# Performance work log

Hardware: AMD Instinct MI355X
Metric: run time of the kernel (lower is better)

The kernel has to match this reference:

```python
import jax, jax.numpy as jnp
import numpy as np

FPFM = 256.0
B = 2097152
C = 32


def _integerize(v, scale):
    # Mirrors ArmInt.set_param_from_float: round-half-away-from-zero to int,
    # stored back as float (pure_int=False path).
    fv = v * scale
    fv = fv + jnp.sign(fv) * 0.5
    return jnp.trunc(fv)  # trunc toward zero == torch .to(int32)


def setup_inputs() -> dict:
    key = jax.random.key(0)
    ks = jax.random.split(key, 8)
    x = jax.random.normal(ks[0], (B, C), dtype=jnp.float32)
    # float-domain params (small, residual-friendly), then integerized
    w0 = _integerize(jax.random.normal(ks[1], (C, C), jnp.float32) * 0.05, FPFM)
    b0 = _integerize(jax.random.normal(ks[2], (C,), jnp.float32) * 0.05, FPFM * FPFM)
    w1 = _integerize(jax.random.normal(ks[3], (C, C), jnp.float32) * 0.05, FPFM)
    b1 = _integerize(jax.random.normal(ks[4], (C,), jnp.float32) * 0.05, FPFM * FPFM)
    w_out = _integerize(jax.random.normal(ks[5], (2, C), jnp.float32) * 0.05, FPFM)
    b_out = _integerize(jax.random.normal(ks[6], (2,), jnp.float32) * 0.05, FPFM * FPFM)
    return {"x": x, "w0": w0, "b0": b0, "w1": w1, "b1": b1,
            "w_out": w_out, "b_out": b_out}


def _arm_layer(h, W, b, residual):
    # F.linear + optional residual scaled by FPFM
    xx = h @ W.T + b
    if residual:
        xx = xx + h * FPFM
    # emulated integer rounding: add sign*FPFM/2, divide, trunc toward zero
    xx = xx + jnp.sign(xx) * (FPFM / 2.0)
    # where(xx<0, -(-xx/f), xx/f) is identity in float; trunc matches .to(int32)
    return jnp.trunc(xx / FPFM)


def reference(x, w0, b0, w1, b1, w_out, b_out):
    h = x * FPFM  # fixed-point lift (pure_int=False: stays float)
    h = jax.nn.relu(_arm_layer(h, w0, b0, True))
    h = jax.nn.relu(_arm_layer(h, w1, b1, True))
    h = _arm_layer(h, w_out, b_out, False)
    raw = h / FPFM  # [B, 2]
    mu = raw[:, 0]
    log_scale = raw[:, 1]
    scale = jnp.exp(jnp.clip(log_scale - 4.0, -4.6, 5.0))
    return mu, scale, log_scale
```

## Files before the change

### kernel.cpp

```cpp
#include <hip/hip_runtime.h>
#include <math.h>


typedef __attribute__((ext_vector_type(8))) short bf16x8;
typedef __attribute__((ext_vector_type(4))) float f32x4;

#define MFMA16(A, B, C) __builtin_amdgcn_mfma_f32_16x16x32_bf16((A), (B), (C), 0, 0, 0)

__device__ inline short bf_top(float v) {
    return (short)(__float_as_uint(v) >> 16);
}
__device__ inline float bf_topf(float v) {
    return __uint_as_float(__float_as_uint(v) & 0xffff0000u);
}


__global__ void armint_prep(const float* __restrict__ w0, const float* __restrict__ b0,
                            const float* __restrict__ w1, const float* __restrict__ b1,
                            const float* __restrict__ wo, const float* __restrict__ bo,
                            short* __restrict__ ws, float* __restrict__ bsf)
{
    int t = threadIdx.x;
    for (int i = t; i < 1024; i += 256) {
        int n = i >> 5, k = i & 31;
        float diag = (n == k) ? 256.0f : 0.0f;

        float a = w0[i] + diag;
        float ahi = bf_topf(a);
        ws[i]          = bf_top(a);
        ws[1024 + i]   = bf_top(a - ahi);

        float b = (w1[i] + diag) * (1.0f / 256.0f);
        float bhi = bf_topf(b);
        ws[2048 + i]   = bf_top(b);
        ws[3072 + i]   = bf_top(b - bhi);

        float c = (n < 2) ? wo[n * 32 + k] * (1.0f / 256.0f) : 0.0f;
        ws[4096 + i]   = bf_top(c);
    }
    if (t < 32) {
        bsf[t]      = (b0[t] + 128.0f) * (1.0f / 256.0f);
        bsf[32 + t] = (b1[t] + 128.0f) * (1.0f / 256.0f);
        bsf[64 + t] = (t < 2) ? bo[t] * (1.0f / 256.0f) : 0.0f;
    }
}

__global__ __launch_bounds__(256)
void armint_mfma(const float* __restrict__ x, const short* __restrict__ ws,
                 const float* __restrict__ bias, float* __restrict__ out, int nrows)
{
    __shared__ float lds_all[4][32 * 36];

    const int lane = threadIdx.x & 63;
    const int wave = threadIdx.x >> 6;
    const int lm   = lane & 15;
    const int quad = lane >> 4;
    float* lds = lds_all[wave];

    const size_t nn = (size_t)nrows;
    const size_t rowbase = (size_t)blockIdx.x * 128 + (size_t)wave * 32;

    bf16x8 w0hi[2], w0lo[2], w1hi[2], w1lo[2], wof;
    float bs0[2], bs1[2];
    #pragma unroll
    for (int hh = 0; hh < 2; ++hh) {
        const int n = lm + 16 * hh;
        const int o = n * 32 + quad * 8;
        w0hi[hh] = *(const bf16x8*)(ws + o);
        w0lo[hh] = *(const bf16x8*)(ws + 1024 + o);
        w1hi[hh] = *(const bf16x8*)(ws + 2048 + o);
        w1lo[hh] = *(const bf16x8*)(ws + 3072 + o);
        bs0[hh] = bias[n];
        bs1[hh] = bias[32 + n];
    }
    wof = *(const bf16x8*)(ws + 4096 + lm * 32 + quad * 8);
    const float bsov = bias[64 + lm];

    bf16x8 a0[2], a1[2], a2[2];
    #pragma unroll
    for (int t = 0; t < 2; ++t) {
        const float* xp = x + (rowbase + (size_t)(t * 16 + lm)) * 32 + quad * 8;
        float4 v0 = *(const float4*)xp;
        float4 v1 = *(const float4*)(xp + 4);
        float h[8] = {v0.x, v0.y, v0.z, v0.w, v1.x, v1.y, v1.z, v1.w};
        #pragma unroll
        for (int j = 0; j < 8; ++j) {
            float c0 = bf_topf(h[j]);
            a0[t][j] = bf_top(h[j]);
            float r1 = h[j] - c0;
            float c1 = bf_topf(r1);
            a1[t][j] = bf_top(r1);
            a2[t][j] = bf_top(r1 - c1);
        }
    }

    f32x4 acc[2][2];
    #pragma unroll
    for (int t = 0; t < 2; ++t)
        #pragma unroll
        for (int hh = 0; hh < 2; ++hh) {
            f32x4 c = {bs0[hh], bs0[hh], bs0[hh], bs0[hh]};
            c = MFMA16(a0[t], w0hi[hh], c);
            c = MFMA16(a1[t], w0hi[hh], c);
            c = MFMA16(a2[t], w0hi[hh], c);
            c = MFMA16(a0[t], w0lo[hh], c);
            c = MFMA16(a1[t], w0lo[hh], c);
            acc[t][hh] = c;
        }
    #pragma unroll
    for (int t = 0; t < 2; ++t)
        #pragma unroll
        for (int hh = 0; hh < 2; ++hh)
            #pragma unroll
            for (int k = 0; k < 4; ++k)
                lds[(t * 16 + quad * 4 + k) * 36 + lm + 16 * hh] =
                    fmaxf(truncf(acc[t][hh][k]), 0.0f);

    bf16x8 c0f[2], c1f[2];
    #pragma unroll
    for (int t = 0; t < 2; ++t) {
        const int base = (t * 16 + lm) * 36 + quad * 8;
        float4 v0 = *(float4*)&lds[base];
        float4 v1 = *(float4*)&lds[base + 4];
        float h[8] = {v0.x, v0.y, v0.z, v0.w, v1.x, v1.y, v1.z, v1.w};
        #pragma unroll
        for (int j = 0; j < 8; ++j) {
            float c0 = bf_topf(h[j]);
            c0f[t][j] = bf_top(h[j]);
            c1f[t][j] = bf_top(h[j] - c0);
        }
    }
    #pragma unroll
    for (int t = 0; t < 2; ++t)
        #pragma unroll
        for (int hh = 0; hh < 2; ++hh) {
            f32x4 c = {bs1[hh], bs1[hh], bs1[hh], bs1[hh]};
            c = MFMA16(c0f[t], w1hi[hh], c);
            c = MFMA16(c1f[t], w1hi[hh], c);
            c = MFMA16(c0f[t], w1lo[hh], c);
            c = MFMA16(c1f[t], w1lo[hh], c);
            acc[t][hh] = c;
        }
    #pragma unroll
    for (int t = 0; t < 2; ++t)
        #pragma unroll
        for (int hh = 0; hh < 2; ++hh)
            #pragma unroll
            for (int k = 0; k < 4; ++k)
                lds[(t * 16 + quad * 4 + k) * 36 + lm + 16 * hh] =
                    fmaxf(truncf(acc[t][hh][k]), 0.0f);

    bf16x8 d0f[2], d1f[2];
    #pragma unroll
    for (int t = 0; t < 2; ++t) {
        const int base = (t * 16 + lm) * 36 + quad * 8;
        float4 v0 = *(float4*)&lds[base];
        float4 v1 = *(float4*)&lds[base + 4];
        float h[8] = {v0.x, v0.y, v0.z, v0.w, v1.x, v1.y, v1.z, v1.w};
        #pragma unroll
        for (int j = 0; j < 8; ++j) {
            float c0 = bf_topf(h[j]);
            d0f[t][j] = bf_top(h[j]);
            d1f[t][j] = bf_top(h[j] - c0);
        }
    }
    #pragma unroll
    for (int t = 0; t < 2; ++t) {
        f32x4 c = {bsov, bsov, bsov, bsov};
        c = MFMA16(d0f[t], wof, c);
        c = MFMA16(d1f[t], wof, c);

        float o[4];
        #pragma unroll
        for (int k = 0; k < 4; ++k) {
            float a = c[k];
            o[k] = truncf(a + copysignf(0.5f, a)) * (1.0f / 256.0f);
        }
        const size_t row = rowbase + (size_t)(t * 16 + quad * 4);
        if (lm == 0) {
            *(float4*)(out + row) = make_float4(o[0], o[1], o[2], o[3]);
        }
        if (lm == 1) {
            *(float4*)(out + 2 * nn + row) = make_float4(o[0], o[1], o[2], o[3]);
            float s[4];
            #pragma unroll
            for (int k = 0; k < 4; ++k)
                s[k] = expf(fminf(fmaxf(o[k] - 4.0f, -4.6f), 5.0f));
            *(float4*)(out + nn + row) = make_float4(s[0], s[1], s[2], s[3]);
        }
    }
}

extern "C" void kernel_launch(void* const* d_in, const int* in_sizes, int n_in,
                              void* d_out, int out_size, void* d_ws, size_t ws_size,
                              hipStream_t stream) {
    const float* x  = (const float*)d_in[0];
    const float* w0 = (const float*)d_in[1];
    const float* b0 = (const float*)d_in[2];
    const float* w1 = (const float*)d_in[3];
    const float* b1 = (const float*)d_in[4];
    const float* wo = (const float*)d_in[5];
    const float* bo = (const float*)d_in[6];
    float* out = (float*)d_out;

    short* ws  = (short*)d_ws;
    float* bsf = (float*)((char*)d_ws + 10240);

    int nrows = in_sizes[0] / 32;
    int grid = nrows / 128;

    armint_prep<<<1, 256, 0, stream>>>(w0, b0, w1, b1, wo, bo, ws, bsf);
    armint_mfma<<<grid, 256, 0, stream>>>(x, ws, bsf, out, nrows);
}
```

Baseline: 372.3 us.

## Process 64 rows per wave, trim bf16 split terms, pack with perm

Each wave now handles 64 rows instead of 32, with all x loads issued up front, and the grid is halved. The input is split into two bf16 parts instead of three, and layers 1 and 2 use three MFMAs per tile instead of five and four, dropping the smaller cross terms. Bf16 packing uses v_perm byte selects to build pairs. Dropping the third split term and the lo×lo products risks rounding mismatches near the trunc boundaries, and the larger per-wave tile raises register and LDS pressure.

```diff
diff --git a/kernel.cpp b/kernel.cpp
--- a/kernel.cpp
+++ b/kernel.cpp
@@ -1,5 +1,6 @@
 #include <hip/hip_runtime.h>
 #include <math.h>
+#include <stdint.h>
 
 
 typedef __attribute__((ext_vector_type(8))) short bf16x8;
@@ -7,11 +8,20 @@
 
 #define MFMA16(A, B, C) __builtin_amdgcn_mfma_f32_16x16x32_bf16((A), (B), (C), 0, 0, 0)
 
+__device__ inline float bf_topf(float v) {
+    return __uint_as_float(__float_as_uint(v) & 0xffff0000u);
+}
 __device__ inline short bf_top(float v) {
     return (short)(__float_as_uint(v) >> 16);
 }
-__device__ inline float bf_topf(float v) {
-    return __uint_as_float(__float_as_uint(v) & 0xffff0000u);
+
+__device__ inline bf16x8 pack_top8(const float f[8]) {
+    union { uint32_t u[4]; bf16x8 v; } r;
+#pragma unroll
+    for (int i = 0; i < 4; ++i)
+        r.u[i] = __builtin_amdgcn_perm(__float_as_uint(f[2 * i + 1]),
+                                       __float_as_uint(f[2 * i]), 0x07060302u);
+    return r.v;
 }
 
 
@@ -26,17 +36,15 @@
         float diag = (n == k) ? 256.0f : 0.0f;
 
         float a = w0[i] + diag;
-        float ahi = bf_topf(a);
-        ws[i]          = bf_top(a);
-        ws[1024 + i]   = bf_top(a - ahi);
+        ws[i]        = bf_top(a);
+        ws[1024 + i] = bf_top(a - bf_topf(a));
 
         float b = (w1[i] + diag) * (1.0f / 256.0f);
-        float bhi = bf_topf(b);
-        ws[2048 + i]   = bf_top(b);
-        ws[3072 + i]   = bf_top(b - bhi);
+        ws[2048 + i] = bf_top(b);
+        ws[3072 + i] = bf_top(b - bf_topf(b));
 
         float c = (n < 2) ? wo[n * 32 + k] * (1.0f / 256.0f) : 0.0f;
-        ws[4096 + i]   = bf_top(c);
+        ws[4096 + i] = bf_top(c);
     }
     if (t < 32) {
         bsf[t]      = (b0[t] + 128.0f) * (1.0f / 256.0f);
@@ -49,20 +57,19 @@
 void armint_mfma(const float* __restrict__ x, const short* __restrict__ ws,
                  const float* __restrict__ bias, float* __restrict__ out, int nrows)
 {
-    __shared__ float lds_all[4][32 * 36];
+    __shared__ float lds_all[4][2][32 * 36];
 
     const int lane = threadIdx.x & 63;
     const int wave = threadIdx.x >> 6;
     const int lm   = lane & 15;
     const int quad = lane >> 4;
-    float* lds = lds_all[wave];
 
     const size_t nn = (size_t)nrows;
-    const size_t rowbase = (size_t)blockIdx.x * 128 + (size_t)wave * 32;
+    const size_t wbase = (size_t)blockIdx.x * 256 + (size_t)wave * 64;
 
     bf16x8 w0hi[2], w0lo[2], w1hi[2], w1lo[2], wof;
     float bs0[2], bs1[2];
-    #pragma unroll
+#pragma unroll
     for (int hh = 0; hh < 2; ++hh) {
         const int n = lm + 16 * hh;
         const int o = n * 32 + quad * 8;
@@ -76,119 +83,129 @@
     wof = *(const bf16x8*)(ws + 4096 + lm * 32 + quad * 8);
     const float bsov = bias[64 + lm];
 
-    bf16x8 a0[2], a1[2], a2[2];
-    #pragma unroll
-    for (int t = 0; t < 2; ++t) {
-        const float* xp = x + (rowbase + (size_t)(t * 16 + lm)) * 32 + quad * 8;
-        float4 v0 = *(const float4*)xp;
-        float4 v1 = *(const float4*)(xp + 4);
-        float h[8] = {v0.x, v0.y, v0.z, v0.w, v1.x, v1.y, v1.z, v1.w};
-        #pragma unroll
-        for (int j = 0; j < 8; ++j) {
-            float c0 = bf_topf(h[j]);
-            a0[t][j] = bf_top(h[j]);
-            float r1 = h[j] - c0;
-            float c1 = bf_topf(r1);
-            a1[t][j] = bf_top(r1);
-            a2[t][j] = bf_top(r1 - c1);
-        }
-    }
-
-    f32x4 acc[2][2];
-    #pragma unroll
-    for (int t = 0; t < 2; ++t)
-        #pragma unroll
-        for (int hh = 0; hh < 2; ++hh) {
-            f32x4 c = {bs0[hh], bs0[hh], bs0[hh], bs0[hh]};
-            c = MFMA16(a0[t], w0hi[hh], c);
-            c = MFMA16(a1[t], w0hi[hh], c);
-            c = MFMA16(a2[t], w0hi[hh], c);
-            c = MFMA16(a0[t], w0lo[hh], c);
-            c = MFMA16(a1[t], w0lo[hh], c);
-            acc[t][hh] = c;
-        }
-    #pragma unroll
-    for (int t = 0; t < 2; ++t)
-        #pragma unroll
-        for (int hh = 0; hh < 2; ++hh)
-            #pragma unroll
-            for (int k = 0; k < 4; ++k)
-                lds[(t * 16 + quad * 4 + k) * 36 + lm + 16 * hh] =
-                    fmaxf(truncf(acc[t][hh][k]), 0.0f);
-
-    bf16x8 c0f[2], c1f[2];
-    #pragma unroll
-    for (int t = 0; t < 2; ++t) {
-        const int base = (t * 16 + lm) * 36 + quad * 8;
-        float4 v0 = *(float4*)&lds[base];
-        float4 v1 = *(float4*)&lds[base + 4];
-        float h[8] = {v0.x, v0.y, v0.z, v0.w, v1.x, v1.y, v1.z, v1.w};
-        #pragma unroll
-        for (int j = 0; j < 8; ++j) {
-            float c0 = bf_topf(h[j]);
-            c0f[t][j] = bf_top(h[j]);
-            c1f[t][j] = bf_top(h[j] - c0);
-        }
-    }
-    #pragma unroll
-    for (int t = 0; t < 2; ++t)
-        #pragma unroll
-        for (int hh = 0; hh < 2; ++hh) {
-            f32x4 c = {bs1[hh], bs1[hh], bs1[hh], bs1[hh]};
-            c = MFMA16(c0f[t], w1hi[hh], c);
-            c = MFMA16(c1f[t], w1hi[hh], c);
-            c = MFMA16(c0f[t], w1lo[hh], c);
-            c = MFMA16(c1f[t], w1lo[hh], c);
-            acc[t][hh] = c;
-        }
-    #pragma unroll
-    for (int t = 0; t < 2; ++t)
-        #pragma unroll
-        for (int hh = 0; hh < 2; ++hh)
-            #pragma unroll
-            for (int k = 0; k < 4; ++k)
-                lds[(t * 16 + quad * 4 + k) * 36 + lm + 16 * hh] =
-                    fmaxf(truncf(acc[t][hh][k]), 0.0f);
-
-    bf16x8 d0f[2], d1f[2];
-    #pragma unroll
-    for (int t = 0; t < 2; ++t) {
-        const int base = (t * 16 + lm) * 36 + quad * 8;
-        float4 v0 = *(float4*)&lds[base];
-        float4 v1 = *(float4*)&lds[base + 4];
-        float h[8] = {v0.x, v0.y, v0.z, v0.w, v1.x, v1.y, v1.z, v1.w};
-        #pragma unroll
-        for (int j = 0; j < 8; ++j) {
-            float c0 = bf_topf(h[j]);
-            d0f[t][j] = bf_top(h[j]);
-            d1f[t][j] = bf_top(h[j] - c0);
-        }
-    }
-    #pragma unroll
-    for (int t = 0; t < 2; ++t) {
-        f32x4 c = {bsov, bsov, bsov, bsov};
-        c = MFMA16(d0f[t], wof, c);
-        c = MFMA16(d1f[t], wof, c);
-
-        float o[4];
-        #pragma unroll
-        for (int k = 0; k < 4; ++k) {
-            float a = c[k];
-            o[k] = truncf(a + copysignf(0.5f, a)) * (1.0f / 256.0f);
-        }
-        const size_t row = rowbase + (size_t)(t * 16 + quad * 4);
-        if (lm == 0) {
-            *(float4*)(out + row) = make_float4(o[0], o[1], o[2], o[3]);
-        }
-        if (lm == 1) {
-            *(float4*)(out + 2 * nn + row) = make_float4(o[0], o[1], o[2], o[3]);
-            float s[4];
-            #pragma unroll
-            for (int k = 0; k < 4; ++k)
-                s[k] = expf(fminf(fmaxf(o[k] - 4.0f, -4.6f), 5.0f));
-            *(float4*)(out + nn + row) = make_float4(s[0], s[1], s[2], s[3]);
-        }
-    }
+    float4 xv[2][2][2];
+#pragma unroll
+    for (int p = 0; p < 2; ++p)
+#pragma unroll
+        for (int t = 0; t < 2; ++t) {
+            const float* xp = x + (wbase + (size_t)(p * 32 + t * 16 + lm)) * 32 + quad * 8;
+            xv[p][t][0] = *(const float4*)xp;
+            xv[p][t][1] = *(const float4*)(xp + 4);
+        }
+
+    bf16x8 a0[2][2], a1[2][2];
+#pragma unroll
+    for (int p = 0; p < 2; ++p)
+#pragma unroll
+        for (int t = 0; t < 2; ++t) {
+            float h[8] = {xv[p][t][0].x, xv[p][t][0].y, xv[p][t][0].z, xv[p][t][0].w,
+                          xv[p][t][1].x, xv[p][t][1].y, xv[p][t][1].z, xv[p][t][1].w};
+            a0[p][t] = pack_top8(h);
+            float r[8];
+#pragma unroll
+            for (int j = 0; j < 8; ++j) r[j] = h[j] - bf_topf(h[j]);
+            a1[p][t] = pack_top8(r);
+        }
+
+    f32x4 acc[2][2][2];
+#pragma unroll
+    for (int p = 0; p < 2; ++p)
+#pragma unroll
+        for (int t = 0; t < 2; ++t)
+#pragma unroll
+            for (int hh = 0; hh < 2; ++hh) {
+                f32x4 c = {bs0[hh], bs0[hh], bs0[hh], bs0[hh]};
+                c = MFMA16(a0[p][t], w0hi[hh], c);
+                c = MFMA16(a1[p][t], w0hi[hh], c);
+                c = MFMA16(a0[p][t], w0lo[hh], c);
+                acc[p][t][hh] = c;
+            }
+#pragma unroll
+    for (int p = 0; p < 2; ++p)
+#pragma unroll
+        for (int t = 0; t < 2; ++t)
+#pragma unroll
+            for (int hh = 0; hh < 2; ++hh)
+#pragma unroll
+                for (int k = 0; k < 4; ++k)
+                    lds_all[wave][p][(t * 16 + quad * 4 + k) * 36 + lm + 16 * hh] =
+                        fmaxf(truncf(acc[p][t][hh][k]), 0.0f);
+
+    bf16x8 c0[2][2], c1[2][2];
+#pragma unroll
+    for (int p = 0; p < 2; ++p)
+#pragma unroll
+        for (int t = 0; t < 2; ++t) {
+            const int base = (t * 16 + lm) * 36 + quad * 8;
+            float4 v0 = *(float4*)&lds_all[wave][p][base];
+            float4 v1 = *(float4*)&lds_all[wave][p][base + 4];
+            float h[8] = {v0.x, v0.y, v0.z, v0.w, v1.x, v1.y, v1.z, v1.w};
+            c0[p][t] = pack_top8(h);
+            float r[8];
+#pragma unroll
+            for (int j = 0; j < 8; ++j) r[j] = h[j] - bf_topf(h[j]);
+            c1[p][t] = pack_top8(r);
+        }
+#pragma unroll
+    for (int p = 0; p < 2; ++p)
+#pragma unroll
+        for (int t = 0; t < 2; ++t)
+#pragma unroll
+            for (int hh = 0; hh < 2; ++hh) {
+                f32x4 c = {bs1[hh], bs1[hh], bs1[hh], bs1[hh]};
+                c = MFMA16(c0[p][t], w1hi[hh], c);
+                c = MFMA16(c1[p][t], w1hi[hh], c);
+                c = MFMA16(c0[p][t], w1lo[hh], c);
+                acc[p][t][hh] = c;
+            }
+#pragma unroll
+    for (int p = 0; p < 2; ++p)
+#pragma unroll
+        for (int t = 0; t < 2; ++t)
+#pragma unroll
+            for (int hh = 0; hh < 2; ++hh)
+#pragma unroll
+                for (int k = 0; k < 4; ++k)
+                    lds_all[wave][p][(t * 16 + quad * 4 + k) * 36 + lm + 16 * hh] =
+                        fmaxf(truncf(acc[p][t][hh][k]), 0.0f);
+
+#pragma unroll
+    for (int p = 0; p < 2; ++p)
+#pragma unroll
+        for (int t = 0; t < 2; ++t) {
+            const int base = (t * 16 + lm) * 36 + quad * 8;
+            float4 v0 = *(float4*)&lds_all[wave][p][base];
+            float4 v1 = *(float4*)&lds_all[wave][p][base + 4];
+            float h[8] = {v0.x, v0.y, v0.z, v0.w, v1.x, v1.y, v1.z, v1.w};
+            bf16x8 d0 = pack_top8(h);
+            float r[8];
+#pragma unroll
+            for (int j = 0; j < 8; ++j) r[j] = h[j] - bf_topf(h[j]);
+            bf16x8 d1 = pack_top8(r);
+
+            f32x4 c = {bsov, bsov, bsov, bsov};
+            c = MFMA16(d0, wof, c);
+            c = MFMA16(d1, wof, c);
+
+            float o[4];
+#pragma unroll
+            for (int k = 0; k < 4; ++k) {
+                float a = c[k];
+                o[k] = truncf(a + copysignf(0.5f, a)) * (1.0f / 256.0f);
+            }
+            const size_t row = wbase + (size_t)(p * 32 + t * 16 + quad * 4);
+            if (lm == 0) {
+                *(float4*)(out + row) = make_float4(o[0], o[1], o[2], o[3]);
+            }
+            if (lm == 1) {
+                *(float4*)(out + 2 * nn + row) = make_float4(o[0], o[1], o[2], o[3]);
+                float s[4];
+#pragma unroll
+                for (int k = 0; k < 4; ++k)
+                    s[k] = expf(fminf(fmaxf(o[k] - 4.0f, -4.6f), 5.0f));
+                *(float4*)(out + nn + row) = make_float4(s[0], s[1], s[2], s[3]);
+            }
+        }
 }
 
 extern "C" void kernel_launch(void* const* d_in, const int* in_sizes, int n_in,
@@ -207,7 +224,7 @@
     float* bsf = (float*)((char*)d_ws + 10240);
 
     int nrows = in_sizes[0] / 32;
-    int grid = nrows / 128;
+    int grid = nrows / 256;
 
     armint_prep<<<1, 256, 0, stream>>>(w0, b0, w1, b1, wo, bo, ws, bsf);
     armint_mfma<<<grid, 256, 0, stream>>>(x, ws, bsf, out, nrows);
```

Result: no change. 374.7 us (+0.6%).
